# Optimization experiments

Hardware: AMD Instinct MI355X
Metric: run time of the kernel (lower is better)

Reference implementation:

```python
import jax, jax.numpy as jnp
import numpy as np

B, H, W, C = 4, 224, 224, 256
HEADS = 8
WIN = 7
N = WIN * WIN  # 49 tokens per window
MLP_HID = 4 * C
EPS = 1e-5


def _rel_index(w):
    coords = np.stack(np.meshgrid(np.arange(w), np.arange(w), indexing='ij'))  # (2,w,w)
    cf = coords.reshape(2, -1)                       # (2, w*w)
    rc = cf[:, :, None] - cf[:, None, :]             # (2, N, N)
    rc = rc.transpose(1, 2, 0).astype(np.int64)      # (N, N, 2)
    rc[:, :, 0] += w - 1
    rc[:, :, 1] += w - 1
    rc[:, :, 0] *= 2 * w - 1
    return jnp.asarray(rc.sum(-1), dtype=jnp.int32)  # (N, N)


def setup_inputs() -> dict:
    key = jax.random.key(0)
    ks = jax.random.split(key, 6)
    std = 0.02
    return {
        'x': jax.random.normal(ks[0], (B, H, W, C), dtype=jnp.float32),
        'norm1_g': jnp.ones((C,), jnp.float32),
        'norm1_b': jnp.zeros((C,), jnp.float32),
        'qkv_w': jax.random.normal(ks[1], (3 * C, C), jnp.float32) * std,
        'qkv_b': jnp.zeros((3 * C,), jnp.float32),
        'bias_table': jax.random.normal(ks[2], ((2 * WIN - 1) ** 2, HEADS), jnp.float32) * std,
        'proj_w': jax.random.normal(ks[3], (C, C), jnp.float32) * std,
        'proj_b': jnp.zeros((C,), jnp.float32),
        'norm2_g': jnp.ones((C,), jnp.float32),
        'norm2_b': jnp.zeros((C,), jnp.float32),
        'fc1_w': jax.random.normal(ks[4], (MLP_HID, C), jnp.float32) * std,
        'fc1_b': jnp.zeros((MLP_HID,), jnp.float32),
        'fc2_w': jax.random.normal(ks[5], (C, MLP_HID), jnp.float32) * std,
        'fc2_b': jnp.zeros((C,), jnp.float32),
        'rel_index': _rel_index(WIN),
    }


def _layernorm(x, g, b):
    mu = jnp.mean(x, axis=-1, keepdims=True)
    var = jnp.mean(jnp.square(x - mu), axis=-1, keepdims=True)
    return (x - mu) * jax.lax.rsqrt(var + EPS) * g + b


def reference(x, norm1_g, norm1_b, qkv_w, qkv_b, bias_table, proj_w, proj_b,
              norm2_g, norm2_b, fc1_w, fc1_b, fc2_w, fc2_b, rel_index):
    Bc, Hc, Wc, Cc = x.shape
    d = Cc // HEADS
    scale = d ** -0.5
    nh, nw = Hc // WIN, Wc // WIN

    shortcut = x
    h = _layernorm(x, norm1_g, norm1_b)

    # window_partition: (B,H,W,C) -> (B*nW, N, C)
    wins = h.reshape(Bc, nh, WIN, nw, WIN, Cc).transpose(0, 1, 3, 2, 4, 5)
    wins = wins.reshape(-1, N, Cc)

    # qkv projection and split into heads
    qkv = wins @ qkv_w.T + qkv_b                                  # (Bw, N, 3C)
    qkv = qkv.reshape(-1, N, 3, HEADS, d).transpose(2, 0, 3, 1, 4)  # (3, Bw, h, N, d)
    q, k, v = qkv[0], qkv[1], qkv[2]

    attn = jnp.einsum('bhnd,bhmd->bhnm', q, k) * scale            # (Bw, h, N, N)
    bias = bias_table[rel_index.reshape(-1)].reshape(N, N, HEADS).transpose(2, 0, 1)
    attn = jax.nn.softmax(attn + bias[None], axis=-1)

    o = jnp.einsum('bhnm,bhmd->bhnd', attn, v)                    # (Bw, h, N, d)
    o = o.transpose(0, 2, 1, 3).reshape(-1, N, Cc)
    o = o @ proj_w.T + proj_b

    # window_reverse: (B*nW, N, C) -> (B,H,W,C)
    o = o.reshape(Bc, nh, nw, WIN, WIN, Cc).transpose(0, 1, 3, 2, 4, 5)
    o = o.reshape(Bc, Hc, Wc, Cc)

    x = shortcut + o
    h2 = _layernorm(x, norm2_g, norm2_b)
    m = jax.nn.gelu(h2 @ fc1_w.T + fc1_b, approximate=False) @ fc2_w.T + fc2_b
    return x + m
```

## Files before the change

### kernel.cpp

```cpp
#include <hip/hip_runtime.h>

typedef unsigned short u16;
typedef __bf16 bf16x8 __attribute__((ext_vector_type(8)));
typedef float f32x4 __attribute__((ext_vector_type(4)));

#define TOKENS 200704
#define QK_ELEMS 51380224UL

__device__ __forceinline__ u16 f2b(float f) {
    __bf16 h = (__bf16)f;
    return __builtin_bit_cast(u16, h);
}

#define GLDS(g, l) __builtin_amdgcn_global_load_lds( \
    (const __attribute__((address_space(1))) void*)(g), \
    (__attribute__((address_space(3))) void*)(l), 16, 0, 0)

#define MFMA __builtin_amdgcn_mfma_f32_16x16x32_bf16

template<int EPI, int WR, int WC>
__global__ __launch_bounds__(512, 4)
void gemm_t(const u16* __restrict__ A, const u16* __restrict__ W,
            const float* __restrict__ bias, int nt, int K,
            u16* __restrict__ outb, float* __restrict__ outf,
            const float* __restrict__ res,
            const float* __restrict__ g2, const float* __restrict__ b2,
            u16* __restrict__ h2o)
{
    constexpr int BM = WR * 64, BN = WC * 64;
    constexpr int ACH = BM / 16;
    constexpr int TCH = (BM + BN) / 16;
    __shared__ u16 As[2][BM * 32];
    __shared__ u16 Bs[2][BN * 32];
    __shared__ float red[EPI == 1 ? 2 * 128 * 4 : 1];

    const int tid  = threadIdx.x;
    const int wave = tid >> 6, lane = tid & 63;

    const int nwg = gridDim.x, bidO = blockIdx.x;
    const int qq = nwg >> 3, rr = nwg & 7;
    const int xcd = bidO & 7, idxx = bidO >> 3;
    const int bid = (xcd < rr) ? (xcd * (qq + 1) + idxx)
                               : (rr * (qq + 1) + (xcd - rr) * qq + idxx);

    const int bm = bid / nt, bn = bid % nt;
    const long m0 = (long)bm * BM;
    const int  n0 = bn * BN;
    const int wr = wave / WC, wc = wave % WC;
    const int lr = lane & 15, lg = lane >> 4;
    const int ccol_s = (((lane & 3) ^ ((lane >> 3) & 3)) * 8);
    const int swzr = (lg ^ ((lr >> 1) & 3)) * 8;

    f32x4 acc[4][4] = {};

    auto stage = [&](int buf, int k0) {
#pragma unroll
        for (int p = 0; p < TCH / 8; ++p) {
            const int q = p * 8 + wave;
            const int rq = (q < ACH) ? q : q - ACH;
            const int row = rq * 16 + (lane >> 2);
            if (q < ACH)
                GLDS(A + (m0 + row) * (long)K + k0 + ccol_s, &As[buf][rq * 512]);
            else
                GLDS(W + (long)(n0 + row) * K + k0 + ccol_s, &Bs[buf][rq * 512]);
        }
    };

    auto compute = [&](int buf) {
        bf16x8 af[4], bfr[4];
#pragma unroll
        for (int fm = 0; fm < 4; ++fm)
            af[fm] = *reinterpret_cast<const bf16x8*>(
                &As[buf][(wr * 64 + fm * 16 + lr) * 32 + swzr]);
#pragma unroll
        for (int fn = 0; fn < 4; ++fn)
            bfr[fn] = *reinterpret_cast<const bf16x8*>(
                &Bs[buf][(wc * 64 + fn * 16 + lr) * 32 + swzr]);
        __builtin_amdgcn_s_setprio(1);
#pragma unroll
        for (int fm = 0; fm < 4; ++fm)
#pragma unroll
            for (int fn = 0; fn < 4; ++fn)
                acc[fm][fn] = MFMA(af[fm], bfr[fn], acc[fm][fn], 0, 0, 0);
        __builtin_amdgcn_s_setprio(0);
    };

    const int nk = K >> 5;
    stage(0, 0);
    stage(1, 32);
    int k = 64;
    for (int t = 0; t < nk; ++t) {
        if (t == nk - 1) asm volatile("s_waitcnt vmcnt(0)" ::: "memory");
        else             asm volatile("s_waitcnt vmcnt(3)" ::: "memory");
        __builtin_amdgcn_s_barrier();
        __builtin_amdgcn_sched_barrier(0);
        compute(t & 1);
        __builtin_amdgcn_s_barrier();
        __builtin_amdgcn_sched_barrier(0);
        if (t + 2 < nk) {
            stage(t & 1, k); k += 32;
            __builtin_amdgcn_sched_barrier(0);
        }
    }

    if constexpr (EPI == 1) {
        float g2c[4], b2c[4];
#pragma unroll
        for (int fn = 0; fn < 4; ++fn) {
            const int n = wc * 64 + fn * 16 + lr;
            g2c[fn] = g2[n]; b2c[fn] = b2[n];
        }
#pragma unroll
        for (int fm = 0; fm < 4; ++fm) {
#pragma unroll
            for (int r = 0; r < 4; ++r) {
                const long m = m0 + wr * 64 + fm * 16 + lg * 4 + r;
                float s = 0.f, s2 = 0.f;
#pragma unroll
                for (int fn = 0; fn < 4; ++fn) {
                    const int n = wc * 64 + fn * 16 + lr;
                    const float x2 = acc[fm][fn][r] + bias[n] + res[m * 256 + n];
                    acc[fm][fn][r] = x2;
                    outf[m * 256 + n] = x2;
                    s += x2; s2 += x2 * x2;
                }
#pragma unroll
                for (int d = 1; d < 16; d <<= 1) { s += __shfl_xor(s, d); s2 += __shfl_xor(s2, d); }
                if (lr == 0) {
                    const int tok = wr * 64 + fm * 16 + lg * 4 + r;
                    red[(0 * 128 + tok) * 4 + wc] = s;
                    red[(1 * 128 + tok) * 4 + wc] = s2;
                }
            }
        }
        __syncthreads();
#pragma unroll
        for (int fm = 0; fm < 4; ++fm) {
#pragma unroll
            for (int r = 0; r < 4; ++r) {
                const int tok = wr * 64 + fm * 16 + lg * 4 + r;
                const float s = red[(0 * 128 + tok) * 4 + 0] + red[(0 * 128 + tok) * 4 + 1]
                              + red[(0 * 128 + tok) * 4 + 2] + red[(0 * 128 + tok) * 4 + 3];
                const float q = red[(1 * 128 + tok) * 4 + 0] + red[(1 * 128 + tok) * 4 + 1]
                              + red[(1 * 128 + tok) * 4 + 2] + red[(1 * 128 + tok) * 4 + 3];
                const float mu = s * 0.00390625f;
                const float rs = rsqrtf(q * 0.00390625f - mu * mu + 1e-5f);
                const long m = m0 + tok;
#pragma unroll
                for (int fn = 0; fn < 4; ++fn) {
                    const int n = wc * 64 + fn * 16 + lr;
                    h2o[m * 256 + n] = f2b((acc[fm][fn][r] - mu) * rs * g2c[fn] + b2c[fn]);
                }
            }
        }
    } else {
#pragma unroll
        for (int fm = 0; fm < 4; ++fm) {
#pragma unroll
            for (int r = 0; r < 4; ++r) {
                const long m = m0 + wr * 64 + fm * 16 + lg * 4 + r;
                size_t mpart = 0;
                if (EPI == 0) {
                    const int gm = (int)m;
                    const int b = gm / 50176;
                    const int rem = gm % 50176;
                    const int y = rem / 224, x = rem % 224;
                    const int win = (b * 32 + y / 7) * 32 + x / 7;
                    const int pos = (y % 7) * 7 + (x % 7);
                    mpart = (size_t)win * 12544 + (size_t)pos * 32;
                }
#pragma unroll
                for (int fn = 0; fn < 4; ++fn) {
                    const int n = n0 + wc * 64 + fn * 16 + lr;
                    const float v = acc[fm][fn][r];
                    if (EPI == 0) {
                        const int sec = n >> 8, hd = (n >> 5) & 7, d = n & 31;
                        const float sc = (sec == 0) ? 0.17677669529663687f : 1.0f;
                        outb[sec * QK_ELEMS + mpart + hd * 1568 + d] = f2b((v + bias[n]) * sc);
                    } else if (EPI == 2) {
                        const float t = v + bias[n];
                        const float s = t * (1.5957691216f + 0.07135481627f * t * t);
                        const float g = t * __builtin_amdgcn_rcpf(1.0f + __expf(-s));
                        outb[m * 1024 + n] = f2b(g);
                    } else {
                        outf[m * 256 + n] += v + bias[n];
                    }
                }
            }
        }
    }
}

__global__ __launch_bounds__(256)
void layernorm_k(const float* __restrict__ in, const float* __restrict__ g,
                 const float* __restrict__ bb, u16* __restrict__ out)
{
    const int token = blockIdx.x * 4 + (threadIdx.x >> 6);
    const int lane = threadIdx.x & 63;
    const float4 v = *reinterpret_cast<const float4*>(in + (size_t)token * 256 + lane * 4);
    float s  = v.x + v.y + v.z + v.w;
    float s2 = v.x * v.x + v.y * v.y + v.z * v.z + v.w * v.w;
#pragma unroll
    for (int m = 1; m < 64; m <<= 1) { s += __shfl_xor(s, m); s2 += __shfl_xor(s2, m); }
    const float mu  = s * (1.0f / 256.0f);
    const float var = s2 * (1.0f / 256.0f) - mu * mu;
    const float rs  = rsqrtf(var + 1e-5f);
    const float4 gv = *reinterpret_cast<const float4*>(g + lane * 4);
    const float4 bv = *reinterpret_cast<const float4*>(bb + lane * 4);
    ushort4 o;
    o.x = f2b((v.x - mu) * rs * gv.x + bv.x);
    o.y = f2b((v.y - mu) * rs * gv.y + bv.y);
    o.z = f2b((v.z - mu) * rs * gv.z + bv.z);
    o.w = f2b((v.w - mu) * rs * gv.w + bv.w);
    *reinterpret_cast<ushort4*>(out + (size_t)token * 256 + lane * 4) = o;
}

__global__ __launch_bounds__(256)
void attn_win(const u16* __restrict__ qkv, const float* __restrict__ biasF,
              u16* __restrict__ outb)
{
    __shared__ u16 plds[4][64 * 72];
    __shared__ u16 vlds[4][32 * 72];
    const int wave = threadIdx.x >> 6, lane = threadIdx.x & 63;
    const int pair = blockIdx.x * 4 + wave;
    const int head = pair & 7, win = pair >> 3;
    const int lr = lane & 15, lg = lane >> 4;

    const u16* Q  = qkv + (size_t)pair * 1568;
    const u16* Kp = qkv + QK_ELEMS + (size_t)pair * 1568;
    const u16* Vp = qkv + 2 * QK_ELEMS + (size_t)pair * 1568;

    u16* vl = &vlds[wave][0];
#pragma unroll
    for (int it = 0; it < 8; ++it) {
        const int idx = it * 64 + lane;
        if (idx < 480) vl[(idx / 15) * 72 + 49 + idx % 15] = 0;
    }
#pragma unroll
    for (int it = 0; it < 4; ++it) {
        const int idx = it * 64 + lane;
        if (idx < 196) {
            const int pos = idx >> 2, dc = idx & 3;
            const uint4 vv = *reinterpret_cast<const uint4*>(Vp + pos * 32 + dc * 8);
            u16* dst = vl + (dc * 8) * 72 + pos;
            dst[0 * 72] = (u16)vv.x;  dst[1 * 72] = (u16)(vv.x >> 16);
            dst[2 * 72] = (u16)vv.y;  dst[3 * 72] = (u16)(vv.y >> 16);
            dst[4 * 72] = (u16)vv.z;  dst[5 * 72] = (u16)(vv.z >> 16);
            dst[6 * 72] = (u16)vv.w;  dst[7 * 72] = (u16)(vv.w >> 16);
        }
    }

    bf16x8 qf[4], kf[4];
#pragma unroll
    for (int f = 0; f < 4; ++f) {
        int n = f * 16 + lr; n = n > 48 ? 48 : n;
        qf[f] = *reinterpret_cast<const bf16x8*>(Q  + n * 32 + lg * 8);
        kf[f] = *reinterpret_cast<const bf16x8*>(Kp + n * 32 + lg * 8);
    }
    f32x4 s[4][4] = {};
#pragma unroll
    for (int fm = 0; fm < 4; ++fm)
#pragma unroll
        for (int fn = 0; fn < 4; ++fn)
            s[fm][fn] = MFMA(qf[fm], kf[fn], s[fm][fn], 0, 0, 0);

    const float* bh = biasF + head * 2401;
    u16* pl = &plds[wave][0];
#pragma unroll
    for (int fm = 0; fm < 4; ++fm) {
#pragma unroll
        for (int r = 0; r < 4; ++r) {
            const int row = fm * 16 + lg * 4 + r;
            const int brow = row > 48 ? 48 : row;
            float v[4];
#pragma unroll
            for (int fn = 0; fn < 4; ++fn) {
                const int col = fn * 16 + lr;
                const float bval = bh[brow * 49 + (col > 48 ? 48 : col)];
                v[fn] = (col > 48) ? -3.0e38f : (s[fm][fn][r] + bval);
            }
            float mx = fmaxf(fmaxf(v[0], v[1]), fmaxf(v[2], v[3]));
#pragma unroll
            for (int d = 1; d < 16; d <<= 1) mx = fmaxf(mx, __shfl_xor(mx, d));
            float p[4], sum = 0.f;
#pragma unroll
            for (int fn = 0; fn < 4; ++fn) {
                const int col = fn * 16 + lr;
                p[fn] = (col <= 48) ? __expf(v[fn] - mx) : 0.f;
                sum += p[fn];
            }
#pragma unroll
            for (int d = 1; d < 16; d <<= 1) sum += __shfl_xor(sum, d);
            const float rinv = __builtin_amdgcn_rcpf(sum);
#pragma unroll
            for (int fn = 0; fn < 4; ++fn)
                pl[row * 72 + fn * 16 + lr] = f2b(p[fn] * rinv);
        }
    }
    __syncthreads();

    f32x4 o[4][2] = {};
#pragma unroll
    for (int kc = 0; kc < 2; ++kc) {
        bf16x8 vf[2];
#pragma unroll
        for (int f2 = 0; f2 < 2; ++f2)
            vf[f2] = *reinterpret_cast<const bf16x8*>(vl + (f2 * 16 + lr) * 72 + kc * 32 + lg * 8);
#pragma unroll
        for (int fm = 0; fm < 4; ++fm) {
            const bf16x8 pa = *reinterpret_cast<const bf16x8*>(pl + (fm * 16 + lr) * 72 + kc * 32 + lg * 8);
#pragma unroll
            for (int f2 = 0; f2 < 2; ++f2)
                o[fm][f2] = MFMA(pa, vf[f2], o[fm][f2], 0, 0, 0);
        }
    }

    const int b = win >> 10, rem = win & 1023, wy = rem >> 5, wx = rem & 31;
#pragma unroll
    for (int fm = 0; fm < 4; ++fm) {
#pragma unroll
        for (int r = 0; r < 4; ++r) {
            const int tok = fm * 16 + lg * 4 + r;
            if (tok > 48) continue;
            const int y = wy * 7 + tok / 7, xx = wx * 7 + tok % 7;
            const size_t mrow = ((size_t)(b * 224 + y)) * 224 + xx;
#pragma unroll
            for (int f2 = 0; f2 < 2; ++f2)
                outb[mrow * 256 + head * 32 + f2 * 16 + lr] = f2b(o[fm][f2][r]);
        }
    }
}

__global__ __launch_bounds__(256)
void cvt_w(const float* __restrict__ qw, const float* __restrict__ pw,
           const float* __restrict__ f1, const float* __restrict__ f2,
           u16* __restrict__ outw)
{
    const int t = blockIdx.x * 256 + threadIdx.x;
    float v;
    if (t < 196608) v = qw[t];
    else if (t < 262144) v = pw[t - 196608];
    else if (t < 524288) v = f1[t - 262144];
    else v = f2[t - 524288];
    outw[t] = f2b(v);
}

__global__ __launch_bounds__(256)
void bias_pre(const float* __restrict__ btab, const int* __restrict__ relidx,
              float* __restrict__ biasF)
{
    const int t = blockIdx.x * 256 + threadIdx.x;
    if (t >= 19208) return;
    const int head = t / 2401, ij = t % 2401;
    biasF[t] = btab[relidx[ij] * 8 + head];
}

extern "C" void kernel_launch(void* const* d_in, const int* in_sizes, int n_in,
                              void* d_out, int out_size, void* d_ws, size_t ws_size,
                              hipStream_t stream)
{
    const float* x      = (const float*)d_in[0];
    const float* n1g    = (const float*)d_in[1];
    const float* n1b    = (const float*)d_in[2];
    const float* qkv_w  = (const float*)d_in[3];
    const float* qkv_b  = (const float*)d_in[4];
    const float* btab   = (const float*)d_in[5];
    const float* proj_w = (const float*)d_in[6];
    const float* proj_b = (const float*)d_in[7];
    const float* n2g    = (const float*)d_in[8];
    const float* n2b    = (const float*)d_in[9];
    const float* fc1_w  = (const float*)d_in[10];
    const float* fc1_b  = (const float*)d_in[11];
    const float* fc2_w  = (const float*)d_in[12];
    const float* fc2_b  = (const float*)d_in[13];
    const int*   relidx = (const int*)d_in[14];
    float* out = (float*)d_out;

    char* ws = (char*)d_ws;
    u16*   wbf   = (u16*)ws;
    float* biasF = (float*)(ws + 1572864);
    u16*   hbuf  = (u16*)(ws + 1650688);
    u16*   rbuf  = (u16*)(ws + 1650688 + 102760448);
    const size_t r_avail = ws_size - (1650688 + 102760448);

    const u16* Wq  = wbf;
    const u16* Wp  = wbf + 196608;
    const u16* Wf1 = wbf + 262144;
    const u16* Wf2 = wbf + 524288;

    cvt_w<<<3072, 256, 0, stream>>>(qkv_w, proj_w, fc1_w, fc2_w, wbf);
    bias_pre<<<76, 256, 0, stream>>>(btab, relidx, biasF);
    layernorm_k<<<50176, 256, 0, stream>>>(x, n1g, n1b, hbuf);

    gemm_t<0, 4, 2><<<784 * 6, 512, 0, stream>>>(hbuf, Wq, qkv_b, 6, 256,
                                                 rbuf, nullptr, nullptr, nullptr, nullptr, nullptr);
    attn_win<<<8192, 256, 0, stream>>>(rbuf, biasF, hbuf);

    gemm_t<1, 2, 4><<<1568, 512, 0, stream>>>(hbuf, Wp, proj_b, 1, 256,
                                              nullptr, out, x, n2g, n2b, hbuf);

    long rows_per = 100352;
    if ((long)(r_avail / 2048) < rows_per) rows_per = 50176;
    for (long r0 = 0; r0 < TOKENS; r0 += rows_per) {
        const long rows = (TOKENS - r0 < rows_per) ? (TOKENS - r0) : rows_per;
        gemm_t<2, 4, 2><<<(int)((rows / 256) * 8), 512, 0, stream>>>(
            hbuf + r0 * 256, Wf1, fc1_b, 8, 256, rbuf, nullptr, nullptr, nullptr, nullptr, nullptr);
        gemm_t<3, 4, 2><<<(int)((rows / 256) * 2), 512, 0, stream>>>(
            rbuf, Wf2, fc2_b, 2, 1024, nullptr, out + r0 * 256, nullptr, nullptr, nullptr, nullptr);
    }
}
```

Before: 1.108 ms.

## Load V via global_load_lds with transposed LDS reads and pre-swizzle bias in MFMA layout

The attention kernel no longer transposes V through scalar 16-bit LDS stores. It issues async global_load_lds copies of V in row layout, overlaps them with the QK MFMA and softmax, and reads transposed fragments with ds_read_b64_tr_b16. The relative-position bias is precomputed per head in the MFMA accumulator layout, with masked columns set to -1e30, so softmax needs one vector load per fragment and no per-element bounds checks. The __syncthreads is replaced by per-wave waitcnts, which is valid only because each wave uses its own LDS slice. The workspace offsets grow to hold the larger bias table.

```diff
diff --git a/kernel.cpp b/kernel.cpp
--- a/kernel.cpp
+++ b/kernel.cpp
@@ -220,7 +220,7 @@
               u16* __restrict__ outb)
 {
     __shared__ u16 plds[4][64 * 72];
-    __shared__ u16 vlds[4][32 * 72];
+    __shared__ u16 vlds[4][2048];
     const int wave = threadIdx.x >> 6, lane = threadIdx.x & 63;
     const int pair = blockIdx.x * 4 + wave;
     const int head = pair & 7, win = pair >> 3;
@@ -230,26 +230,6 @@
     const u16* Kp = qkv + QK_ELEMS + (size_t)pair * 1568;
     const u16* Vp = qkv + 2 * QK_ELEMS + (size_t)pair * 1568;
 
-    u16* vl = &vlds[wave][0];
-#pragma unroll
-    for (int it = 0; it < 8; ++it) {
-        const int idx = it * 64 + lane;
-        if (idx < 480) vl[(idx / 15) * 72 + 49 + idx % 15] = 0;
-    }
-#pragma unroll
-    for (int it = 0; it < 4; ++it) {
-        const int idx = it * 64 + lane;
-        if (idx < 196) {
-            const int pos = idx >> 2, dc = idx & 3;
-            const uint4 vv = *reinterpret_cast<const uint4*>(Vp + pos * 32 + dc * 8);
-            u16* dst = vl + (dc * 8) * 72 + pos;
-            dst[0 * 72] = (u16)vv.x;  dst[1 * 72] = (u16)(vv.x >> 16);
-            dst[2 * 72] = (u16)vv.y;  dst[3 * 72] = (u16)(vv.y >> 16);
-            dst[4 * 72] = (u16)vv.z;  dst[5 * 72] = (u16)(vv.z >> 16);
-            dst[6 * 72] = (u16)vv.w;  dst[7 * 72] = (u16)(vv.w >> 16);
-        }
-    }
-
     bf16x8 qf[4], kf[4];
 #pragma unroll
     for (int f = 0; f < 4; ++f) {
@@ -257,6 +237,19 @@
         qf[f] = *reinterpret_cast<const bf16x8*>(Q  + n * 32 + lg * 8);
         kf[f] = *reinterpret_cast<const bf16x8*>(Kp + n * 32 + lg * 8);
     }
+
+    u16* vl = &vlds[wave][0];
+    {
+        const int posh = lane >> 1, dsub = (lane & 1) * 8;
+#pragma unroll
+        for (int db = 0; db < 2; ++db)
+#pragma unroll
+            for (int half = 0; half < 2; ++half) {
+                int pos = half * 32 + posh; if (pos > 48) pos = 48;
+                GLDS(Vp + pos * 32 + db * 16 + dsub, vl + db * 1024 + half * 512);
+            }
+    }
+
     f32x4 s[4][4] = {};
 #pragma unroll
     for (int fm = 0; fm < 4; ++fm)
@@ -264,54 +257,75 @@
         for (int fn = 0; fn < 4; ++fn)
             s[fm][fn] = MFMA(qf[fm], kf[fn], s[fm][fn], 0, 0, 0);
 
-    const float* bh = biasF + head * 2401;
+    const float* bfh = biasF + head * 4096;
     u16* pl = &plds[wave][0];
 #pragma unroll
     for (int fm = 0; fm < 4; ++fm) {
+        f32x4 bb[4];
+#pragma unroll
+        for (int fn = 0; fn < 4; ++fn)
+            bb[fn] = *reinterpret_cast<const f32x4*>(bfh + ((fm * 4 + fn) << 8) + (lane << 2));
 #pragma unroll
         for (int r = 0; r < 4; ++r) {
             const int row = fm * 16 + lg * 4 + r;
-            const int brow = row > 48 ? 48 : row;
-            float v[4];
-#pragma unroll
-            for (int fn = 0; fn < 4; ++fn) {
-                const int col = fn * 16 + lr;
-                const float bval = bh[brow * 49 + (col > 48 ? 48 : col)];
-                v[fn] = (col > 48) ? -3.0e38f : (s[fm][fn][r] + bval);
-            }
-            float mx = fmaxf(fmaxf(v[0], v[1]), fmaxf(v[2], v[3]));
+            float v0 = s[fm][0][r] + bb[0][r];
+            float v1 = s[fm][1][r] + bb[1][r];
+            float v2 = s[fm][2][r] + bb[2][r];
+            float v3 = s[fm][3][r] + bb[3][r];
+            float mx = fmaxf(fmaxf(v0, v1), fmaxf(v2, v3));
 #pragma unroll
             for (int d = 1; d < 16; d <<= 1) mx = fmaxf(mx, __shfl_xor(mx, d));
-            float p[4], sum = 0.f;
-#pragma unroll
-            for (int fn = 0; fn < 4; ++fn) {
-                const int col = fn * 16 + lr;
-                p[fn] = (col <= 48) ? __expf(v[fn] - mx) : 0.f;
-                sum += p[fn];
-            }
+            const float p0 = __expf(v0 - mx), p1 = __expf(v1 - mx);
+            const float p2 = __expf(v2 - mx), p3 = __expf(v3 - mx);
+            float sum = p0 + p1 + p2 + p3;
 #pragma unroll
             for (int d = 1; d < 16; d <<= 1) sum += __shfl_xor(sum, d);
             const float rinv = __builtin_amdgcn_rcpf(sum);
-#pragma unroll
-            for (int fn = 0; fn < 4; ++fn)
-                pl[row * 72 + fn * 16 + lr] = f2b(p[fn] * rinv);
-        }
-    }
-    __syncthreads();
+            pl[row * 72 +  0 + lr] = f2b(p0 * rinv);
+            pl[row * 72 + 16 + lr] = f2b(p1 * rinv);
+            pl[row * 72 + 32 + lr] = f2b(p2 * rinv);
+            pl[row * 72 + 48 + lr] = f2b(p3 * rinv);
+        }
+    }
+
+    asm volatile("s_waitcnt vmcnt(0)" ::: "memory");
+    if (lane < 60) {
+        const int db = lane / 30, ix = lane % 30;
+        f32x4 z = {0.f, 0.f, 0.f, 0.f};
+        *reinterpret_cast<f32x4*>(vl + db * 1024 + 784 + ix * 8) = z;
+    }
+    asm volatile("s_waitcnt lgkmcnt(0)" ::: "memory");
+    __builtin_amdgcn_sched_barrier(0);
+
+    const unsigned VB = (unsigned)(unsigned long)
+        (__attribute__((address_space(3))) u16*)vl;
+    unsigned long long trv[2][2][2];
+#pragma unroll
+    for (int kc = 0; kc < 2; ++kc)
+#pragma unroll
+        for (int f2 = 0; f2 < 2; ++f2) {
+            const unsigned va = VB + f2 * 2048 + kc * 1024 + lg * 256 + lr * 2;
+            asm volatile("ds_read_b64_tr_b16 %0, %1"
+                         : "=v"(trv[kc][f2][0]) : "v"(va));
+            asm volatile("ds_read_b64_tr_b16 %0, %1 offset:128"
+                         : "=v"(trv[kc][f2][1]) : "v"(va));
+        }
+    asm volatile("s_waitcnt lgkmcnt(0)" ::: "memory");
+    __builtin_amdgcn_sched_barrier(0);
 
     f32x4 o[4][2] = {};
 #pragma unroll
     for (int kc = 0; kc < 2; ++kc) {
-        bf16x8 vf[2];
-#pragma unroll
-        for (int f2 = 0; f2 < 2; ++f2)
-            vf[f2] = *reinterpret_cast<const bf16x8*>(vl + (f2 * 16 + lr) * 72 + kc * 32 + lg * 8);
 #pragma unroll
         for (int fm = 0; fm < 4; ++fm) {
-            const bf16x8 pa = *reinterpret_cast<const bf16x8*>(pl + (fm * 16 + lr) * 72 + kc * 32 + lg * 8);
-#pragma unroll
-            for (int f2 = 0; f2 < 2; ++f2)
-                o[fm][f2] = MFMA(pa, vf[f2], o[fm][f2], 0, 0, 0);
+            const bf16x8 pa = *reinterpret_cast<const bf16x8*>(
+                pl + (fm * 16 + lr) * 72 + kc * 32 + lg * 8);
+#pragma unroll
+            for (int f2 = 0; f2 < 2; ++f2) {
+                union { unsigned long long q[2]; bf16x8 v; } u;
+                u.q[0] = trv[kc][f2][0]; u.q[1] = trv[kc][f2][1];
+                o[fm][f2] = MFMA(pa, u.v, o[fm][f2], 0, 0, 0);
+            }
         }
     }
 
@@ -350,9 +364,18 @@
               float* __restrict__ biasF)
 {
     const int t = blockIdx.x * 256 + threadIdx.x;
-    if (t >= 19208) return;
-    const int head = t / 2401, ij = t % 2401;
-    biasF[t] = btab[relidx[ij] * 8 + head];
+    const int head = t >> 10, rem = t & 1023;
+    const int fr = rem >> 6, lane = rem & 63;
+    const int fm = fr >> 2, fn = fr & 3;
+    const int lr = lane & 15, lg = lane >> 4;
+    const int col = fn * 16 + lr;
+    f32x4 o;
+#pragma unroll
+    for (int r = 0; r < 4; ++r) {
+        int row = fm * 16 + lg * 4 + r; if (row > 48) row = 48;
+        o[r] = (col > 48) ? -1e30f : btab[relidx[row * 49 + col] * 8 + head];
+    }
+    *reinterpret_cast<f32x4*>(biasF + t * 4) = o;
 }
 
 extern "C" void kernel_launch(void* const* d_in, const int* in_sizes, int n_in,
@@ -379,9 +402,9 @@
     char* ws = (char*)d_ws;
     u16*   wbf   = (u16*)ws;
     float* biasF = (float*)(ws + 1572864);
-    u16*   hbuf  = (u16*)(ws + 1650688);
-    u16*   rbuf  = (u16*)(ws + 1650688 + 102760448);
-    const size_t r_avail = ws_size - (1650688 + 102760448);
+    u16*   hbuf  = (u16*)(ws + 1703936);
+    u16*   rbuf  = (u16*)(ws + 1703936 + 102760448);
+    const size_t r_avail = ws_size - (1703936 + 102760448);
 
     const u16* Wq  = wbf;
     const u16* Wp  = wbf + 196608;
@@ -389,7 +412,7 @@
     const u16* Wf2 = wbf + 524288;
 
     cvt_w<<<3072, 256, 0, stream>>>(qkv_w, proj_w, fc1_w, fc2_w, wbf);
-    bias_pre<<<76, 256, 0, stream>>>(btab, relidx, biasF);
+    bias_pre<<<32, 256, 0, stream>>>(btab, relidx, biasF);
     layernorm_k<<<50176, 256, 0, stream>>>(x, n1g, n1b, hbuf);
 
     gemm_t<0, 4, 2><<<784 * 6, 512, 0, stream>>>(hbuf, Wq, qkv_b, 6, 256,
```

Measured after the change: 1.001 ms. -9.7%, faster.
